# Kernel tuning notes

Hardware: AMD Instinct MI355X
Metric: run time of the kernel (lower is better)

Reference implementation:

```python
import jax, jax.numpy as jnp
import numpy as np

N = 32768          # nodes
DEG = 16           # fixed in-degree per dst node
E = N * DEG        # edges
IN_FEATS = 256
HEADS = 4
OUT = 64
NUM_CLASSES = 40
SLOPE = 0.2        # leaky_relu negative slope
GM = 0.1           # graph margin
CM = 0.1           # class margin


def setup_inputs() -> dict:
    key = jax.random.key(0)
    ks = jax.random.split(key, 8)
    feat = jax.random.normal(ks[0], (N, IN_FEATS), dtype=jnp.float32)
    label = jax.random.randint(ks[1], (N,), 0, NUM_CLASSES)
    src = jax.random.randint(ks[2], (E,), 0, N)
    # dst sorted with fixed in-degree DEG -> dense mailboxes of shape [N, DEG, ...]
    dst = jnp.repeat(jnp.arange(N), DEG)
    # negative graph: same src, dst permuted (construct_negative_graph, k=1)
    neg_perm = jax.random.permutation(ks[3], E)
    scale_w = (2.0 / (IN_FEATS + HEADS * OUT)) ** 0.5  # xavier-ish
    W = jax.random.normal(ks[4], (HEADS * OUT, IN_FEATS), dtype=jnp.float32) * scale_w
    scale_a = (2.0 / (1 + OUT)) ** 0.5
    attn_l = jax.random.normal(ks[5], (HEADS, OUT), dtype=jnp.float32) * scale_a
    attn_r = jax.random.normal(ks[6], (HEADS, OUT), dtype=jnp.float32) * scale_a
    return {"feat": feat, "label": label, "src": src, "dst": dst,
            "neg_perm": neg_perm, "W": W, "attn_l": attn_l, "attn_r": attn_r}


def _leaky(x):
    return jnp.where(x >= 0, x, SLOPE * x)


def reference(feat, label, src, dst, neg_perm, W, attn_l, attn_r):
    n = feat.shape[0]
    e_count = src.shape[0]
    deg = e_count // n
    H, D = attn_l.shape

    feat_src = (feat @ W.T).reshape(n, H, D)               # [N,H,D]
    el = jnp.einsum('nhd,hd->nh', feat_src, attn_l)        # [N,H]
    er = jnp.einsum('nhd,hd->nh', feat_src, attn_r)        # [N,H]
    e = _leaky(el[src] + er[dst])                          # [E,H]

    # ---- graph loss (negative sampling margin) ----
    neg_dst = dst[neg_perm]
    ne = _leaky(el[src] + er[neg_dst])                     # [E,H]
    pw = e.reshape(n, deg, H)                              # positive msgs per dst
    nw = ne.reshape(n, deg, H)                             # negative msgs per dst
    Lg = jnp.maximum(nw[:, :, None, :] + GM - pw[:, None, :, :], 0.0).sum() / (n * H)

    # ---- boundary (class) loss: same-label vs diff-label neighbors ----
    adj = (label[src] == label[dst]).reshape(n, deg)       # [N,DEG] bool
    # difference[n,a,b,h] = w[n,b,h] + CM - w[n,a,h], valid iff adj[a] & ~adj[b]
    val = jnp.maximum(pw[:, None, :, :] + CM - pw[:, :, None, :], 0.0)
    mask = (adj[:, :, None] & (~adj[:, None, :]))[..., None]
    Lb = jnp.where(mask, val, 0.0).sum() / (n * H)

    # ---- edge softmax over each dst's in-edges + attention-weighted sum ----
    a = jax.nn.softmax(pw, axis=1)                         # [N,DEG,H]
    ft = feat_src[src].reshape(n, deg, H, D)               # gathered src feats
    rst = jnp.einsum('ndh,ndhf->nhf', a, ft)               # [N,H,D]
    return rst, Lg, Lb
```

## Files before the change

### kernel.cpp

```cpp
#include <hip/hip_runtime.h>
#include <hip/hip_bf16.h>

#define N_NODES 32768
#define DEG 16
#define E_EDGES (N_NODES * DEG)
#define HEADS 4
#define OUT_D 64
#define HD 256
#define SLOPE 0.2f
#define GMARG 0.1f
#define CMARG 0.1f
#define LOSS_BLOCKS 2048

typedef float f32x4 __attribute__((ext_vector_type(4)));
typedef unsigned short ushort4v __attribute__((ext_vector_type(4)));
typedef short bf16x8 __attribute__((ext_vector_type(8)));
typedef short short4v __attribute__((ext_vector_type(4)));

__device__ __forceinline__ float bf2f(unsigned short u) {
    return __uint_as_float(((unsigned int)u) << 16);
}
__device__ __forceinline__ unsigned short f2bf(float x) {
    __hip_bfloat16 h = __float2bfloat16(x);
    return __builtin_bit_cast(unsigned short, h);
}
__device__ __forceinline__ short f2bf_s(float x) {
    __hip_bfloat16 h = __float2bfloat16(x);
    return __builtin_bit_cast(short, h);
}
__device__ __forceinline__ float leaky(float x) {
    return x >= 0.f ? x : SLOPE * x;
}

__global__ void badcfg_kernel(float* out, float code) {
    out[0] = code;
}

__global__ __launch_bounds__(256) void convw_kernel(const float* __restrict__ W,
                                                    short* __restrict__ Wb) {
    const int i = (blockIdx.x * 256 + threadIdx.x) * 4;
    f32x4 v = *(const f32x4*)(W + i);
    short4v o;
    o[0] = f2bf_s(v[0]); o[1] = f2bf_s(v[1]); o[2] = f2bf_s(v[2]); o[3] = f2bf_s(v[3]);
    *(short4v*)(Wb + i) = o;
}

__global__ __launch_bounds__(256) void gemm_kernel(const float* __restrict__ feat,
                                                   const short* __restrict__ Wb,
                                                   const float* __restrict__ attn_l,
                                                   const float* __restrict__ attn_r,
                                                   unsigned short* __restrict__ fsb,
                                                   float* __restrict__ el,
                                                   float* __restrict__ er) {
    __shared__ short s_b[16384];
    __shared__ float s_al[128], s_ar[128];

    const int tid = threadIdx.x;
    const int node_tile = blockIdx.x >> 1;
    const int colhalf = blockIdx.x & 1;
    const int colbase = colhalf * 128;

    if (tid < 128) {
        s_al[tid] = attn_l[colbase + tid];
        s_ar[tid] = attn_r[colbase + tid];
    }

    const int wave = tid >> 6;
    const int lane = tid & 63;
    const int row0 = (node_tile * 4 + wave) * 16;
    const int m = lane & 15;
    const int q = lane >> 4;

    bf16x8 afr[8];
    const float* arow = feat + (size_t)(row0 + m) * HD + q * 8;
#pragma unroll
    for (int kk = 0; kk < 8; ++kk) {
        f32x4 lo = *(const f32x4*)(arow + kk * 32);
        f32x4 hi = *(const f32x4*)(arow + kk * 32 + 4);
        bf16x8 a;
        a[0] = f2bf_s(lo[0]); a[1] = f2bf_s(lo[1]); a[2] = f2bf_s(lo[2]); a[3] = f2bf_s(lo[3]);
        a[4] = f2bf_s(hi[0]); a[5] = f2bf_s(hi[1]); a[6] = f2bf_s(hi[2]); a[7] = f2bf_s(hi[3]);
        afr[kk] = a;
    }

    f32x4 acc[8];
#pragma unroll
    for (int t = 0; t < 8; ++t) acc[t] = (f32x4)(0.0f);

#pragma unroll
    for (int khalf = 0; khalf < 2; ++khalf) {
        __syncthreads();
#pragma unroll
        for (int it = 0; it < 8; ++it) {
            const int u = it * 256 + tid;
            const int c_local = u >> 4;
            const int kg = u & 15;
            const int t_l = c_local >> 4;
            const int mm = c_local & 15;
            const int c32 = kg >> 2;
            const int qq = kg & 3;
            const int kelem = khalf * 128 + c32 * 32 + qq * 8;
            bf16x8 v = *(const bf16x8*)(Wb + (size_t)(colbase + c_local) * HD + kelem);
            *(bf16x8*)(s_b + (((c32 * 8 + t_l) * 64) + qq * 16 + mm) * 8) = v;
        }
        __syncthreads();

#pragma unroll
        for (int c32 = 0; c32 < 4; ++c32) {
            const bf16x8 af = afr[khalf * 4 + c32];
#pragma unroll
            for (int t = 0; t < 8; ++t) {
                bf16x8 bfr = *(const bf16x8*)(s_b + (((c32 * 8 + t) * 64) + lane) * 8);
                acc[t] = __builtin_amdgcn_mfma_f32_16x16x32_bf16(af, bfr, acc[t], 0, 0, 0);
            }
        }
    }

#pragma unroll
    for (int t = 0; t < 8; ++t) {
#pragma unroll
        for (int r = 0; r < 4; ++r) {
            fsb[(size_t)(row0 + q * 4 + r) * HD + colbase + t * 16 + m] = f2bf(acc[t][r]);
        }
    }

    float pel[2][4], per_[2][4];
#pragma unroll
    for (int hl = 0; hl < 2; ++hl)
#pragma unroll
        for (int r = 0; r < 4; ++r) { pel[hl][r] = 0.f; per_[hl][r] = 0.f; }
#pragma unroll
    for (int t = 0; t < 8; ++t) {
        const float al = s_al[t * 16 + m];
        const float ar = s_ar[t * 16 + m];
        const int hl = t >> 2;
#pragma unroll
        for (int r = 0; r < 4; ++r) {
            pel[hl][r] += acc[t][r] * al;
            per_[hl][r] += acc[t][r] * ar;
        }
    }
#pragma unroll
    for (int mask = 1; mask < 16; mask <<= 1) {
#pragma unroll
        for (int hl = 0; hl < 2; ++hl)
#pragma unroll
            for (int r = 0; r < 4; ++r) {
                pel[hl][r] += __shfl_xor(pel[hl][r], mask, 64);
                per_[hl][r] += __shfl_xor(per_[hl][r], mask, 64);
            }
    }
    if (m < 8) {
        const int hl = m >> 2, r = m & 3;
        const int hg = colhalf * 2 + hl;
        const int node = row0 + q * 4 + r;
        const float vel = (hl == 0) ? pel[0][r] : pel[1][r];
        const float ver = (hl == 0) ? per_[0][r] : per_[1][r];
        el[node * 4 + hg] = vel;
        er[node * 4 + hg] = ver;
    }
}

__global__ __launch_bounds__(256) void loss_kernel(const int* __restrict__ src,
                                                   const int* __restrict__ perm,
                                                   const int* __restrict__ label,
                                                   const float* __restrict__ el,
                                                   const float* __restrict__ er,
                                                   float* __restrict__ partials) {
    __shared__ float s_pw[16][16][4];
    __shared__ int   s_adj[16][16];
    __shared__ float slg[4], slb[4];

    const int tid = threadIdx.x;
    const int wave = tid >> 6;
    const int lane = tid & 63;
    const int w = lane >> 4;
    const int a = lane & 15;
    const int nl = wave * 4 + w;
    const int n = blockIdx.x * 16 + nl;
    const int e = n * DEG + a;

    const int s  = src[e];
    const int nd = perm[e] >> 4;
    f32x4 els  = *(const f32x4*)(el + (size_t)s * 4);
    f32x4 ern  = *(const f32x4*)(er + (size_t)n * 4);
    f32x4 ernd = *(const f32x4*)(er + (size_t)nd * 4);
    const int adja = (label[s] == label[n]) ? 1 : 0;

    f32x4 pw, nw;
#pragma unroll
    for (int h = 0; h < 4; ++h) {
        pw[h] = leaky(els[h] + ern[h]);
        nw[h] = leaky(els[h] + ernd[h]);
    }
    *(f32x4*)&s_pw[nl][a][0] = pw;
    s_adj[nl][a] = adja;
    __syncthreads();

    float lg = 0.f, lb = 0.f;
#pragma unroll
    for (int b = 0; b < 16; ++b) {
        f32x4 pwb = *(const f32x4*)&s_pw[nl][b][0];
        const int adjb = s_adj[nl][b];
#pragma unroll
        for (int h = 0; h < 4; ++h)
            lg += fmaxf(nw[h] + GMARG - pwb[h], 0.f);
        if (adja && !adjb) {
#pragma unroll
            for (int h = 0; h < 4; ++h)
                lb += fmaxf(pwb[h] + CMARG - pw[h], 0.f);
        }
    }
#pragma unroll
    for (int mask = 1; mask < 64; mask <<= 1) {
        lg += __shfl_xor(lg, mask, 64);
        lb += __shfl_xor(lb, mask, 64);
    }
    if (lane == 0) { slg[wave] = lg; slb[wave] = lb; }
    __syncthreads();
    if (tid == 0) {
        partials[blockIdx.x * 2]     = slg[0] + slg[1] + slg[2] + slg[3];
        partials[blockIdx.x * 2 + 1] = slb[0] + slb[1] + slb[2] + slb[3];
    }
}

__global__ __launch_bounds__(256) void aggregate_kernel(const int* __restrict__ src,
                                                        const float* __restrict__ el,
                                                        const float* __restrict__ er,
                                                        const unsigned short* __restrict__ fsb,
                                                        float* __restrict__ out) {
    __shared__ float a_sm[4][64];
    __shared__ int sidx[4][16];
    const int tid = threadIdx.x;
    const int wave = tid >> 6;
    const int lane = tid & 63;
    const int n = blockIdx.x * 4 + wave;

    if (lane < DEG) sidx[wave][lane] = src[n * DEG + lane];
    __syncthreads();

    {
        const int j = lane >> 2, h = lane & 3;
        float a = leaky(el[sidx[wave][j] * 4 + h] + er[n * 4 + h]);
        float mx = a;
#pragma unroll
        for (int mask = 4; mask < 64; mask <<= 1)
            mx = fmaxf(mx, __shfl_xor(mx, mask, 64));
        float ee = __expf(a - mx);
        float s = ee;
#pragma unroll
        for (int mask = 4; mask < 64; mask <<= 1)
            s += __shfl_xor(s, mask, 64);
        a_sm[wave][lane] = ee / s;
    }
    __syncthreads();

    const int h2 = lane >> 4;
    f32x4 acc = (f32x4)(0.f);
#pragma unroll
    for (int j = 0; j < DEG; ++j) {
        const float aw = a_sm[wave][j * 4 + h2];
        ushort4v u = *(const ushort4v*)(fsb + (size_t)sidx[wave][j] * HD + lane * 4);
        acc[0] += aw * bf2f(u[0]);
        acc[1] += aw * bf2f(u[1]);
        acc[2] += aw * bf2f(u[2]);
        acc[3] += aw * bf2f(u[3]);
    }
    *(f32x4*)(out + (size_t)n * HD + lane * 4) = acc;
}

__global__ __launch_bounds__(256) void finalize_kernel(const float* __restrict__ partials,
                                                       float* __restrict__ out) {
    const int tid = threadIdx.x;
    const int lane = tid & 63;
    const int wave = tid >> 6;
    double lg = 0.0, lb = 0.0;
    for (int i = tid; i < LOSS_BLOCKS; i += 256) {
        lg += (double)partials[i * 2];
        lb += (double)partials[i * 2 + 1];
    }
#pragma unroll
    for (int mask = 1; mask < 64; mask <<= 1) {
        lg += __shfl_xor(lg, mask, 64);
        lb += __shfl_xor(lb, mask, 64);
    }
    __shared__ double slg[4], slb[4];
    if (lane == 0) { slg[wave] = lg; slb[wave] = lb; }
    __syncthreads();
    if (tid == 0) {
        const double scale = 1.0 / (double)((size_t)N_NODES * HEADS);
        out[(size_t)N_NODES * HD]     = (float)((slg[0] + slg[1] + slg[2] + slg[3]) * scale);
        out[(size_t)N_NODES * HD + 1] = (float)((slb[0] + slb[1] + slb[2] + slb[3]) * scale);
    }
}

extern "C" void kernel_launch(void* const* d_in, const int* in_sizes, int n_in,
                              void* d_out, int out_size, void* d_ws, size_t ws_size,
                              hipStream_t stream) {
    const float* feat   = (const float*)d_in[0];
    const int*   label  = (const int*)d_in[1];
    const int*   src    = (const int*)d_in[2];
    const int*   perm   = (const int*)d_in[4];
    const float* W      = (const float*)d_in[5];
    const float* attn_l = (const float*)d_in[6];
    const float* attn_r = (const float*)d_in[7];
    float* out = (float*)d_out;

    const int expect[8] = {8388608, 32768, 524288, 524288, 524288, 65536, 256, 256};
    if (n_in != 8) {
        hipLaunchKernelGGL(badcfg_kernel, dim3(1), dim3(1), 0, stream, out, 60000.f);
        return;
    }
    for (int i = 0; i < 8; ++i) {
        if (in_sizes[i] != expect[i]) {
            hipLaunchKernelGGL(badcfg_kernel, dim3(1), dim3(1), 0, stream, out,
                               65536.f + 256.f * (float)i);
            return;
        }
    }
    if (out_size != N_NODES * HD + 2) {
        hipLaunchKernelGGL(badcfg_kernel, dim3(1), dim3(1), 0, stream, out, 200000.f);
        return;
    }

    char* ws = (char*)d_ws;
    size_t off = 0;
    float* partials = (float*)(ws + off); off += (size_t)LOSS_BLOCKS * 2 * sizeof(float);
    off = (off + 255) & ~(size_t)255;
    short* Wb = (short*)(ws + off); off += (size_t)HD * HD * sizeof(short);
    off = (off + 255) & ~(size_t)255;
    unsigned short* fsb = (unsigned short*)(ws + off); off += (size_t)N_NODES * HD * sizeof(unsigned short);
    float* el = (float*)(ws + off); off += (size_t)N_NODES * HEADS * sizeof(float);
    float* er = (float*)(ws + off); off += (size_t)N_NODES * HEADS * sizeof(float);
    if (off > ws_size) {
        hipLaunchKernelGGL(badcfg_kernel, dim3(1), dim3(1), 0, stream, out, 131072.f);
        return;
    }

    hipLaunchKernelGGL(convw_kernel, dim3(HD * HD / 1024), dim3(256), 0, stream, W, Wb);
    hipLaunchKernelGGL(gemm_kernel, dim3(N_NODES / 64 * 2), dim3(256), 0, stream,
                       feat, Wb, attn_l, attn_r, fsb, el, er);
    hipLaunchKernelGGL(loss_kernel, dim3(LOSS_BLOCKS), dim3(256), 0, stream,
                       src, perm, label, el, er, partials);
    hipLaunchKernelGGL(aggregate_kernel, dim3(N_NODES / 4), dim3(256), 0, stream,
                       src, el, er, fsb, out);
    hipLaunchKernelGGL(finalize_kernel, dim3(1), dim3(256), 0, stream, partials, out);
}
```

Measured before the change: 171.2 us.

## Fuse loss and aggregation kernels; widen GEMM to full columns with async LDS double-buffering

```diff
diff --git a/kernel.cpp b/kernel.cpp
--- a/kernel.cpp
+++ b/kernel.cpp
@@ -14,6 +14,7 @@
 
 typedef float f32x4 __attribute__((ext_vector_type(4)));
 typedef unsigned short ushort4v __attribute__((ext_vector_type(4)));
+typedef unsigned short ushort8v __attribute__((ext_vector_type(8)));
 typedef short bf16x8 __attribute__((ext_vector_type(8)));
 typedef short short4v __attribute__((ext_vector_type(4)));
 
@@ -30,6 +31,11 @@
 }
 __device__ __forceinline__ float leaky(float x) {
     return x >= 0.f ? x : SLOPE * x;
+}
+__device__ __forceinline__ void gl_lds16(const void* g, void* l) {
+    __builtin_amdgcn_global_load_lds(
+        (__attribute__((address_space(1))) void*)(g),
+        (__attribute__((address_space(3))) void*)(l), 16, 0, 0);
 }
 
 __global__ void badcfg_kernel(float* out, float code) {
@@ -52,24 +58,22 @@
                                                    unsigned short* __restrict__ fsb,
                                                    float* __restrict__ el,
                                                    float* __restrict__ er) {
-    __shared__ short s_b[16384];
-    __shared__ float s_al[128], s_ar[128];
+    __shared__ short s_b[2][16384];
 
     const int tid = threadIdx.x;
-    const int node_tile = blockIdx.x >> 1;
-    const int colhalf = blockIdx.x & 1;
-    const int colbase = colhalf * 128;
-
-    if (tid < 128) {
-        s_al[tid] = attn_l[colbase + tid];
-        s_ar[tid] = attn_r[colbase + tid];
-    }
-
     const int wave = tid >> 6;
     const int lane = tid & 63;
-    const int row0 = (node_tile * 4 + wave) * 16;
+    const int row0 = (blockIdx.x * 4 + wave) * 16;
     const int m = lane & 15;
     const int q = lane >> 4;
+
+#pragma unroll
+    for (int i = 0; i < 8; ++i) {
+        const int sb = wave * 8 + i;
+        const int kk2 = sb >> 4, t = sb & 15;
+        const short* g = Wb + (size_t)(t * 16 + m) * HD + kk2 * 32 + q * 8;
+        gl_lds16(g, &s_b[0][sb * 512]);
+    }
 
     bf16x8 afr[8];
     const float* arow = feat + (size_t)(row0 + m) * HD + q * 8;
@@ -77,98 +81,101 @@
     for (int kk = 0; kk < 8; ++kk) {
         f32x4 lo = *(const f32x4*)(arow + kk * 32);
         f32x4 hi = *(const f32x4*)(arow + kk * 32 + 4);
-        bf16x8 a;
-        a[0] = f2bf_s(lo[0]); a[1] = f2bf_s(lo[1]); a[2] = f2bf_s(lo[2]); a[3] = f2bf_s(lo[3]);
-        a[4] = f2bf_s(hi[0]); a[5] = f2bf_s(hi[1]); a[6] = f2bf_s(hi[2]); a[7] = f2bf_s(hi[3]);
-        afr[kk] = a;
-    }
-
-    f32x4 acc[8];
-#pragma unroll
-    for (int t = 0; t < 8; ++t) acc[t] = (f32x4)(0.0f);
-
-#pragma unroll
-    for (int khalf = 0; khalf < 2; ++khalf) {
-        __syncthreads();
-#pragma unroll
-        for (int it = 0; it < 8; ++it) {
-            const int u = it * 256 + tid;
-            const int c_local = u >> 4;
-            const int kg = u & 15;
-            const int t_l = c_local >> 4;
-            const int mm = c_local & 15;
-            const int c32 = kg >> 2;
-            const int qq = kg & 3;
-            const int kelem = khalf * 128 + c32 * 32 + qq * 8;
-            bf16x8 v = *(const bf16x8*)(Wb + (size_t)(colbase + c_local) * HD + kelem);
-            *(bf16x8*)(s_b + (((c32 * 8 + t_l) * 64) + qq * 16 + mm) * 8) = v;
-        }
-        __syncthreads();
-
-#pragma unroll
-        for (int c32 = 0; c32 < 4; ++c32) {
-            const bf16x8 af = afr[khalf * 4 + c32];
-#pragma unroll
-            for (int t = 0; t < 8; ++t) {
-                bf16x8 bfr = *(const bf16x8*)(s_b + (((c32 * 8 + t) * 64) + lane) * 8);
+        bf16x8 aa;
+        aa[0] = f2bf_s(lo[0]); aa[1] = f2bf_s(lo[1]); aa[2] = f2bf_s(lo[2]); aa[3] = f2bf_s(lo[3]);
+        aa[4] = f2bf_s(hi[0]); aa[5] = f2bf_s(hi[1]); aa[6] = f2bf_s(hi[2]); aa[7] = f2bf_s(hi[3]);
+        afr[kk] = aa;
+    }
+
+    f32x4 acc[16];
+#pragma unroll
+    for (int t = 0; t < 16; ++t) acc[t] = (f32x4)(0.0f);
+
+    __syncthreads();
+
+#pragma unroll
+    for (int c = 0; c < 4; ++c) {
+        if (c < 3) {
+#pragma unroll
+            for (int i = 0; i < 8; ++i) {
+                const int sb = wave * 8 + i;
+                const int kk2 = sb >> 4, t = sb & 15;
+                const short* g = Wb + (size_t)(t * 16 + m) * HD + (c + 1) * 64 + kk2 * 32 + q * 8;
+                gl_lds16(g, &s_b[(c + 1) & 1][sb * 512]);
+            }
+        }
+        const short* sbc = s_b[c & 1];
+#pragma unroll
+        for (int kk2 = 0; kk2 < 2; ++kk2) {
+            const bf16x8 af = afr[c * 2 + kk2];
+#pragma unroll
+            for (int t = 0; t < 16; ++t) {
+                bf16x8 bfr = *(const bf16x8*)(sbc + ((kk2 * 16 + t) * 64 + lane) * 8);
                 acc[t] = __builtin_amdgcn_mfma_f32_16x16x32_bf16(af, bfr, acc[t], 0, 0, 0);
             }
         }
-    }
-
-#pragma unroll
-    for (int t = 0; t < 8; ++t) {
+        __syncthreads();
+    }
+
+#pragma unroll
+    for (int t = 0; t < 16; ++t) {
 #pragma unroll
         for (int r = 0; r < 4; ++r) {
-            fsb[(size_t)(row0 + q * 4 + r) * HD + colbase + t * 16 + m] = f2bf(acc[t][r]);
-        }
-    }
-
-    float pel[2][4], per_[2][4];
-#pragma unroll
-    for (int hl = 0; hl < 2; ++hl)
-#pragma unroll
-        for (int r = 0; r < 4; ++r) { pel[hl][r] = 0.f; per_[hl][r] = 0.f; }
-#pragma unroll
-    for (int t = 0; t < 8; ++t) {
-        const float al = s_al[t * 16 + m];
-        const float ar = s_ar[t * 16 + m];
-        const int hl = t >> 2;
+            fsb[(size_t)(row0 + q * 4 + r) * HD + t * 16 + m] = f2bf(acc[t][r]);
+        }
+    }
+
+    float pel[4][4], per_[4][4];
+#pragma unroll
+    for (int h = 0; h < 4; ++h)
+#pragma unroll
+        for (int r = 0; r < 4; ++r) { pel[h][r] = 0.f; per_[h][r] = 0.f; }
+#pragma unroll
+    for (int t = 0; t < 16; ++t) {
+        const float al = attn_l[t * 16 + m];
+        const float ar = attn_r[t * 16 + m];
+        const int h = t >> 2;
 #pragma unroll
         for (int r = 0; r < 4; ++r) {
-            pel[hl][r] += acc[t][r] * al;
-            per_[hl][r] += acc[t][r] * ar;
+            pel[h][r] += acc[t][r] * al;
+            per_[h][r] += acc[t][r] * ar;
         }
     }
 #pragma unroll
     for (int mask = 1; mask < 16; mask <<= 1) {
 #pragma unroll
-        for (int hl = 0; hl < 2; ++hl)
+        for (int h = 0; h < 4; ++h)
 #pragma unroll
             for (int r = 0; r < 4; ++r) {
-                pel[hl][r] += __shfl_xor(pel[hl][r], mask, 64);
-                per_[hl][r] += __shfl_xor(per_[hl][r], mask, 64);
+                pel[h][r] += __shfl_xor(pel[h][r], mask, 64);
+                per_[h][r] += __shfl_xor(per_[h][r], mask, 64);
             }
     }
-    if (m < 8) {
-        const int hl = m >> 2, r = m & 3;
-        const int hg = colhalf * 2 + hl;
-        const int node = row0 + q * 4 + r;
-        const float vel = (hl == 0) ? pel[0][r] : pel[1][r];
-        const float ver = (hl == 0) ? per_[0][r] : per_[1][r];
-        el[node * 4 + hg] = vel;
-        er[node * 4 + hg] = ver;
-    }
-}
-
-__global__ __launch_bounds__(256) void loss_kernel(const int* __restrict__ src,
-                                                   const int* __restrict__ perm,
-                                                   const int* __restrict__ label,
-                                                   const float* __restrict__ el,
-                                                   const float* __restrict__ er,
-                                                   float* __restrict__ partials) {
-    __shared__ float s_pw[16][16][4];
-    __shared__ int   s_adj[16][16];
+    if (m == 0) {
+#pragma unroll
+        for (int r = 0; r < 4; ++r) {
+            const int node = row0 + q * 4 + r;
+            f32x4 vl, vr;
+            vl[0] = pel[0][r]; vl[1] = pel[1][r]; vl[2] = pel[2][r]; vl[3] = pel[3][r];
+            vr[0] = per_[0][r]; vr[1] = per_[1][r]; vr[2] = per_[2][r]; vr[3] = per_[3][r];
+            *(f32x4*)(el + (size_t)node * 4) = vl;
+            *(f32x4*)(er + (size_t)node * 4) = vr;
+        }
+    }
+}
+
+__global__ __launch_bounds__(256) void fla_kernel(const int* __restrict__ src,
+                                                  const int* __restrict__ perm,
+                                                  const int* __restrict__ label,
+                                                  const float* __restrict__ el,
+                                                  const float* __restrict__ er,
+                                                  const unsigned short* __restrict__ fsb,
+                                                  float* __restrict__ out,
+                                                  float* __restrict__ partials) {
+    __shared__ float s_pw[16][17][4];
+    __shared__ float s_a[16][17][4];
+    __shared__ int   s_adj[16][17];
+    __shared__ int   s_srcn[16][17];
     __shared__ float slg[4], slb[4];
 
     const int tid = threadIdx.x;
@@ -195,6 +202,26 @@
     }
     *(f32x4*)&s_pw[nl][a][0] = pw;
     s_adj[nl][a] = adja;
+    s_srcn[nl][a] = s;
+
+    f32x4 mx = pw;
+#pragma unroll
+    for (int mask = 1; mask < 16; mask <<= 1)
+#pragma unroll
+        for (int h = 0; h < 4; ++h)
+            mx[h] = fmaxf(mx[h], __shfl_xor(mx[h], mask, 64));
+    f32x4 ee, sm;
+#pragma unroll
+    for (int h = 0; h < 4; ++h) { ee[h] = __expf(pw[h] - mx[h]); sm[h] = ee[h]; }
+#pragma unroll
+    for (int mask = 1; mask < 16; mask <<= 1)
+#pragma unroll
+        for (int h = 0; h < 4; ++h)
+            sm[h] += __shfl_xor(sm[h], mask, 64);
+    f32x4 aw;
+#pragma unroll
+    for (int h = 0; h < 4; ++h) aw[h] = ee[h] / sm[h];
+    *(f32x4*)&s_a[nl][a][0] = aw;
     __syncthreads();
 
     float lg = 0.f, lb = 0.f;
@@ -222,51 +249,33 @@
         partials[blockIdx.x * 2]     = slg[0] + slg[1] + slg[2] + slg[3];
         partials[blockIdx.x * 2 + 1] = slb[0] + slb[1] + slb[2] + slb[3];
     }
-}
-
-__global__ __launch_bounds__(256) void aggregate_kernel(const int* __restrict__ src,
-                                                        const float* __restrict__ el,
-                                                        const float* __restrict__ er,
-                                                        const unsigned short* __restrict__ fsb,
-                                                        float* __restrict__ out) {
-    __shared__ float a_sm[4][64];
-    __shared__ int sidx[4][16];
-    const int tid = threadIdx.x;
-    const int wave = tid >> 6;
-    const int lane = tid & 63;
-    const int n = blockIdx.x * 4 + wave;
-
-    if (lane < DEG) sidx[wave][lane] = src[n * DEG + lane];
-    __syncthreads();
-
-    {
-        const int j = lane >> 2, h = lane & 3;
-        float a = leaky(el[sidx[wave][j] * 4 + h] + er[n * 4 + h]);
-        float mx = a;
-#pragma unroll
-        for (int mask = 4; mask < 64; mask <<= 1)
-            mx = fmaxf(mx, __shfl_xor(mx, mask, 64));
-        float ee = __expf(a - mx);
-        float s = ee;
-#pragma unroll
-        for (int mask = 4; mask < 64; mask <<= 1)
-            s += __shfl_xor(s, mask, 64);
-        a_sm[wave][lane] = ee / s;
-    }
-    __syncthreads();
-
-    const int h2 = lane >> 4;
-    f32x4 acc = (f32x4)(0.f);
-#pragma unroll
-    for (int j = 0; j < DEG; ++j) {
-        const float aw = a_sm[wave][j * 4 + h2];
-        ushort4v u = *(const ushort4v*)(fsb + (size_t)sidx[wave][j] * HD + lane * 4);
-        acc[0] += aw * bf2f(u[0]);
-        acc[1] += aw * bf2f(u[1]);
-        acc[2] += aw * bf2f(u[2]);
-        acc[3] += aw * bf2f(u[3]);
-    }
-    *(f32x4*)(out + (size_t)n * HD + lane * 4) = acc;
+
+    const int nl2 = tid >> 4;
+    const int tt  = tid & 15;
+    const int hh  = tt >> 2;
+    const int n2  = blockIdx.x * 16 + nl2;
+    float acc[16];
+#pragma unroll
+    for (int k = 0; k < 16; ++k) acc[k] = 0.f;
+#pragma unroll 4
+    for (int j = 0; j < 16; ++j) {
+        const int s2 = s_srcn[nl2][j];
+        const float awj = s_a[nl2][j][hh];
+        const unsigned short* rp = fsb + (size_t)s2 * HD + tt * 16;
+        ushort8v u0 = *(const ushort8v*)(rp);
+        ushort8v u1 = *(const ushort8v*)(rp + 8);
+#pragma unroll
+        for (int k = 0; k < 8; ++k) acc[k]     += awj * bf2f(u0[k]);
+#pragma unroll
+        for (int k = 0; k < 8; ++k) acc[8 + k] += awj * bf2f(u1[k]);
+    }
+    float* op = out + (size_t)n2 * HD + tt * 16;
+#pragma unroll
+    for (int i = 0; i < 4; ++i) {
+        f32x4 v;
+        v[0] = acc[i * 4]; v[1] = acc[i * 4 + 1]; v[2] = acc[i * 4 + 2]; v[3] = acc[i * 4 + 3];
+        *(f32x4*)(op + i * 4) = v;
+    }
 }
 
 __global__ __launch_bounds__(256) void finalize_kernel(const float* __restrict__ partials,
@@ -338,11 +347,9 @@
     }
 
     hipLaunchKernelGGL(convw_kernel, dim3(HD * HD / 1024), dim3(256), 0, stream, W, Wb);
-    hipLaunchKernelGGL(gemm_kernel, dim3(N_NODES / 64 * 2), dim3(256), 0, stream,
+    hipLaunchKernelGGL(gemm_kernel, dim3(N_NODES / 64), dim3(256), 0, stream,
                        feat, Wb, attn_l, attn_r, fsb, el, er);
-    hipLaunchKernelGGL(loss_kernel, dim3(LOSS_BLOCKS), dim3(256), 0, stream,
-                       src, perm, label, el, er, partials);
-    hipLaunchKernelGGL(aggregate_kernel, dim3(N_NODES / 4), dim3(256), 0, stream,
-                       src, el, er, fsb, out);
+    hipLaunchKernelGGL(fla_kernel, dim3(LOSS_BLOCKS), dim3(256), 0, stream,
+                       src, perm, label, el, er, fsb, out, partials);
     hipLaunchKernelGGL(finalize_kernel, dim3(1), dim3(256), 0, stream, partials, out);
 }
```

Measured after the change: 156.8 us (median of 3 runs). -8.4%, faster.
